# Optimization experiments

Measured on AMD Instinct MI355X. Metric: run time of the kernel, lower is better.

## Reference

```python
import jax, jax.numpy as jnp
import numpy as np

N = 40000      # nodes
E = 640000     # edges (avg degree 16)
F_IN = 32      # input node feature dim
G = 64         # graphs in batch
DIMS = [(F_IN, 128), (128, 64), (64, 32), (32, 16)]


def setup_inputs() -> dict:
    key = jax.random.key(0)
    ks = jax.random.split(key, 16)
    inp = {
        "x": jax.random.normal(ks[0], (N, F_IN), jnp.float32),
        "edge_index": jax.random.randint(ks[1], (2, E), 0, N),
        "batch": jnp.sort(jax.random.randint(ks[2], (N,), 0, G)),
    }
    k = 3
    for i, (din, dout) in enumerate(DIMS, 1):
        s = 1.0 / np.sqrt(din)
        inp[f"W{i}_rel"] = jax.random.uniform(ks[k], (din, dout), jnp.float32, -s, s); k += 1
        inp[f"b{i}"] = jax.random.uniform(ks[k], (dout,), jnp.float32, -s, s); k += 1
        inp[f"W{i}_root"] = jax.random.uniform(ks[k], (din, dout), jnp.float32, -s, s); k += 1
    s = 1.0 / np.sqrt(16)
    inp["Wfc"] = jax.random.uniform(ks[15], (16, 1), jnp.float32, -s, s)
    inp["bfc"] = jax.random.uniform(jax.random.fold_in(key, 99), (1,), jnp.float32, -s, s)
    return inp


def _graph_conv(x, src, dst, W_rel, b, W_root):
    # PyG GraphConv (aggr='add'): out_i = (sum_{j->i} x_j) @ W_rel + b + x_i @ W_root
    agg = jax.ops.segment_sum(x[src], dst, num_segments=N)  # gather -> scatter-add
    return agg @ W_rel + b + x @ W_root


def reference(x, edge_index, batch,
              W1_rel, b1, W1_root, W2_rel, b2, W2_root,
              W3_rel, b3, W3_root, W4_rel, b4, W4_root, Wfc, bfc):
    src, dst = edge_index[0], edge_index[1]
    h = jax.nn.relu(_graph_conv(x, src, dst, W1_rel, b1, W1_root))
    h = jax.nn.relu(_graph_conv(h, src, dst, W2_rel, b2, W2_root))
    h = jax.nn.relu(_graph_conv(h, src, dst, W3_rel, b3, W3_root))
    h = _graph_conv(h, src, dst, W4_rel, b4, W4_root)  # no ReLU before pooling
    # global mean pool per graph
    sums = jax.ops.segment_sum(h, batch, num_segments=G)                       # [G, 16]
    counts = jax.ops.segment_sum(jnp.ones((N, 1), h.dtype), batch, num_segments=G)
    pooled = sums / jnp.maximum(counts, 1.0)
    return pooled @ Wfc + bfc  # [G, 1]
```

## Files before the change

### kernel.cpp

```cpp
#include <hip/hip_runtime.h>

#define NN 40000
#define NE 640000
#define NG 64
#define SCAN_NB ((NN + 255) / 256)
#define CCAP 768

typedef unsigned short ushort_t;

__device__ __forceinline__ float fcomp(const float4& v, int t) {
    return t == 0 ? v.x : t == 1 ? v.y : t == 2 ? v.z : v.w;
}
__device__ __forceinline__ unsigned int pack2bf(float a, float b) {
    unsigned int ua = __float_as_uint(a);
    unsigned int ub = __float_as_uint(b);
    ua = (ua + 0x7fffu + ((ua >> 16) & 1u)) >> 16;
    ub = (ub + 0x7fffu + ((ub >> 16) & 1u)) >> 16;
    return ua | (ub << 16);
}
__device__ __forceinline__ uint2 pack4bf(const float4& v) {
    return make_uint2(pack2bf(v.x, v.y), pack2bf(v.z, v.w));
}
__device__ __forceinline__ float lo2f(unsigned int u) { return __uint_as_float(u << 16); }
__device__ __forceinline__ float hi2f(unsigned int u) { return __uint_as_float(u & 0xffff0000u); }
__device__ __forceinline__ void acc8(const uint4& u, float4& lo, float4& hi) {
    lo.x += lo2f(u.x); lo.y += hi2f(u.x); lo.z += lo2f(u.y); lo.w += hi2f(u.y);
    hi.x += lo2f(u.z); hi.y += hi2f(u.z); hi.z += lo2f(u.w); hi.w += hi2f(u.w);
}
typedef __attribute__((ext_vector_type(2))) float f32x2;
__device__ __forceinline__ unsigned int pack4fp8(const float4& v) {
    unsigned int r = 0;
    r = __builtin_amdgcn_cvt_pk_fp8_f32(v.x, v.y, r, false);
    r = __builtin_amdgcn_cvt_pk_fp8_f32(v.z, v.w, r, true);
    return r;
}
__device__ __forceinline__ void accf8x4(unsigned int u, float4& a) {
    f32x2 lo = __builtin_amdgcn_cvt_pk_f32_fp8(u, false);
    f32x2 hi = __builtin_amdgcn_cvt_pk_f32_fp8(u, true);
    a.x += lo[0]; a.y += lo[1]; a.z += hi[0]; a.w += hi[1];
}

__global__ __launch_bounds__(256) void prep_kernel(
        int* __restrict__ zp, int nz,
        const float4* __restrict__ x4,
        uint2* __restrict__ xb,
        const float* __restrict__ W4rel,
        const float* __restrict__ W4root,
        const float* __restrict__ b4,
        const float* __restrict__ Wfc,
        float* __restrict__ wf) {
    int i = blockIdx.x * 256 + threadIdx.x;
    if (i < nz) zp[i] = 0;
    if (i < NN * 8) { float4 v = x4[i]; xb[i] = pack4bf(v); }
    if (blockIdx.x == 0) {
        int t = threadIdx.x;
        if (t < 32) {
            float a = 0.f, b = 0.f;
#pragma unroll
            for (int j = 0; j < 16; ++j) {
                float w = Wfc[j];
                a += W4rel[t * 16 + j] * w;
                b += W4root[t * 16 + j] * w;
            }
            wf[t] = a;
            wf[32 + t] = b;
        } else if (t == 32) {
            float s = 0.f;
#pragma unroll
            for (int j = 0; j < 16; ++j) s += b4[j] * Wfc[j];
            wf[64] = s;
        }
    }
}

__global__ void hist_kernel(const int* __restrict__ dst, int* __restrict__ deg,
                            int* __restrict__ epos) {
    int e = blockIdx.x * blockDim.x + threadIdx.x;
    if (e < NE) epos[e] = atomicAdd(&deg[dst[e]], 1);
}

__global__ __launch_bounds__(256) void scan1_kernel(const int* __restrict__ deg,
                                                    int* __restrict__ rowptr,
                                                    int* __restrict__ bsum) {
    __shared__ int ws[4];
    __shared__ int wpre[4];
    int i = blockIdx.x * 256 + threadIdx.x;
    int lane = threadIdx.x & 63, wid = threadIdx.x >> 6;
    int v = (i < NN) ? deg[i] : 0;
    int incl = v;
#pragma unroll
    for (int off = 1; off < 64; off <<= 1) {
        int u = __shfl_up(incl, off, 64);
        if (lane >= off) incl += u;
    }
    if (lane == 63) ws[wid] = incl;
    __syncthreads();
    if (threadIdx.x == 0) {
        int s = 0;
#pragma unroll
        for (int w = 0; w < 4; ++w) { wpre[w] = s; s += ws[w]; }
        bsum[blockIdx.x] = s;
    }
    __syncthreads();
    if (i < NN) rowptr[i] = wpre[wid] + (incl - v);
}

__global__ __launch_bounds__(256) void scan23_kernel(int* __restrict__ rowptr,
                                                     const int* __restrict__ bsum) {
    __shared__ int ws[4];
    int t = threadIdx.x, b = blockIdx.x;
    int v = (t < b) ? bsum[t] : 0;
#pragma unroll
    for (int off = 32; off; off >>= 1) v += __shfl_xor(v, off, 64);
    if ((t & 63) == 0) ws[t >> 6] = v;
    __syncthreads();
    int soff = ws[0] + ws[1] + ws[2] + ws[3];
    int i = b * 256 + t;
    if (i < NN) rowptr[i] += soff;
    if (b == SCAN_NB - 1 && t == 0) rowptr[NN] = soff + bsum[b];
}

__global__ void fill_kernel(const int* __restrict__ src, const int* __restrict__ dst,
                            const int* __restrict__ rowptr, const int* __restrict__ epos,
                            ushort_t* __restrict__ col) {
    int e = blockIdx.x * blockDim.x + threadIdx.x;
    if (e < NE) col[rowptr[dst[e]] + epos[e]] = (ushort_t)src[e];
}

__global__ __launch_bounds__(256, 4) void fconv1_kernel(
        const uint4* __restrict__ xb4,
        const float4* __restrict__ x,
        const int* __restrict__ rowptr,
        const ushort_t* __restrict__ col,
        const float4* __restrict__ Wrel,
        const float4* __restrict__ Wroot,
        const float4* __restrict__ bias,
        float4* __restrict__ out) {
    __shared__ float4 sA[32][9];
    __shared__ float4 sR[32 * 32];
    __shared__ float4 sT[32 * 32];
    __shared__ ushort_t scol[CCAP];
    int t = threadIdx.x;
    for (int i = t; i < 32 * 32; i += 256) { sR[i] = Wrel[i]; sT[i] = Wroot[i]; }
    int blk0 = blockIdx.x * 32;
    int ebeg = rowptr[blk0], eend = rowptr[blk0 + 32];
    bool gat = t < 128;
    int na = t >> 2, c = t & 3;
    int node = blk0 + (gat ? na : 0);
    int beg = gat ? rowptr[node] : 0;
    int end = gat ? rowptr[node + 1] : 0;
    float4 aLo = {0.f, 0.f, 0.f, 0.f}, aHi = {0.f, 0.f, 0.f, 0.f};
    for (int base = ebeg; base < eend; base += CCAP) {
        int cnt = eend - base < CCAP ? eend - base : CCAP;
        __syncthreads();
        for (int i = t; i < cnt; i += 256) scol[i] = col[base + i];
        __syncthreads();
        if (gat) {
            int lo = beg > base ? beg : base;
            int hi = end < base + cnt ? end : base + cnt;
            int e = lo;
            for (; e + 4 <= hi; e += 4) {
                uint4 u0 = xb4[(size_t)scol[e - base] * 4 + c];
                uint4 u1 = xb4[(size_t)scol[e - base + 1] * 4 + c];
                uint4 u2 = xb4[(size_t)scol[e - base + 2] * 4 + c];
                uint4 u3 = xb4[(size_t)scol[e - base + 3] * 4 + c];
                acc8(u0, aLo, aHi); acc8(u1, aLo, aHi);
                acc8(u2, aLo, aHi); acc8(u3, aLo, aHi);
            }
            for (; e < hi; ++e) {
                uint4 u = xb4[(size_t)scol[e - base] * 4 + c];
                acc8(u, aLo, aHi);
            }
        }
    }
    if (gat) { sA[na][2 * c] = aLo; sA[na][2 * c + 1] = aHi; }
    __syncthreads();
    int jg = t % 16, mg = t / 16;
    int n0 = blk0 + mg * 2;
    float4 bb0 = bias[2 * jg], bb1 = bias[2 * jg + 1];
    float4 acc00 = bb0, acc01 = bb1, acc10 = bb0, acc11 = bb1;
#pragma unroll 2
    for (int kc = 0; kc < 8; ++kc) {
        float4 a0 = sA[2 * mg][kc];
        float4 a1 = sA[2 * mg + 1][kc];
        float4 x0 = x[(size_t)n0 * 8 + kc];
        float4 x1 = x[(size_t)(n0 + 1) * 8 + kc];
#pragma unroll
        for (int tt = 0; tt < 4; ++tt) {
            int k = kc * 4 + tt;
            float4 wr0 = sR[k * 32 + 2 * jg], wr1 = sR[k * 32 + 2 * jg + 1];
            float4 wt0 = sT[k * 32 + 2 * jg], wt1 = sT[k * 32 + 2 * jg + 1];
            float av0 = fcomp(a0, tt), xv0 = fcomp(x0, tt);
            float av1 = fcomp(a1, tt), xv1 = fcomp(x1, tt);
            acc00.x += av0 * wr0.x + xv0 * wt0.x;
            acc00.y += av0 * wr0.y + xv0 * wt0.y;
            acc00.z += av0 * wr0.z + xv0 * wt0.z;
            acc00.w += av0 * wr0.w + xv0 * wt0.w;
            acc01.x += av0 * wr1.x + xv0 * wt1.x;
            acc01.y += av0 * wr1.y + xv0 * wt1.y;
            acc01.z += av0 * wr1.z + xv0 * wt1.z;
            acc01.w += av0 * wr1.w + xv0 * wt1.w;
            acc10.x += av1 * wr0.x + xv1 * wt0.x;
            acc10.y += av1 * wr0.y + xv1 * wt0.y;
            acc10.z += av1 * wr0.z + xv1 * wt0.z;
            acc10.w += av1 * wr0.w + xv1 * wt0.w;
            acc11.x += av1 * wr1.x + xv1 * wt1.x;
            acc11.y += av1 * wr1.y + xv1 * wt1.y;
            acc11.z += av1 * wr1.z + xv1 * wt1.z;
            acc11.w += av1 * wr1.w + xv1 * wt1.w;
        }
    }
    float4 r;
    r.x = fmaxf(acc00.x, 0.f); r.y = fmaxf(acc00.y, 0.f);
    r.z = fmaxf(acc00.z, 0.f); r.w = fmaxf(acc00.w, 0.f);
    out[(size_t)n0 * 32 + 2 * jg] = r;
    r.x = fmaxf(acc01.x, 0.f); r.y = fmaxf(acc01.y, 0.f);
    r.z = fmaxf(acc01.z, 0.f); r.w = fmaxf(acc01.w, 0.f);
    out[(size_t)n0 * 32 + 2 * jg + 1] = r;
    r.x = fmaxf(acc10.x, 0.f); r.y = fmaxf(acc10.y, 0.f);
    r.z = fmaxf(acc10.z, 0.f); r.w = fmaxf(acc10.w, 0.f);
    out[(size_t)(n0 + 1) * 32 + 2 * jg] = r;
    r.x = fmaxf(acc11.x, 0.f); r.y = fmaxf(acc11.y, 0.f);
    r.z = fmaxf(acc11.z, 0.f); r.w = fmaxf(acc11.w, 0.f);
    out[(size_t)(n0 + 1) * 32 + 2 * jg + 1] = r;
}

__global__ __launch_bounds__(256, 6) void mmyz_kernel(
        const float4* __restrict__ h,
        const float4* __restrict__ Wrel,
        const float4* __restrict__ Wroot,
        const float4* __restrict__ bias,
        unsigned int* __restrict__ y2f8,
        float4* __restrict__ z2) {
    __shared__ float4 sR[32 * 16];
    __shared__ float4 sT[32 * 16];
    int jl = threadIdx.x % 16;
    int mg = threadIdx.x / 16;
    int n0 = blockIdx.x * 32 + mg * 2;
    float4 bb = bias[jl];
    float4 ay0 = {0.f, 0.f, 0.f, 0.f}, ay1 = {0.f, 0.f, 0.f, 0.f};
    float4 az0 = bb, az1 = bb;
    for (int s = 0; s < 4; ++s) {
        if (s) __syncthreads();
        for (int i = threadIdx.x; i < 512; i += 256) {
            sR[i] = Wrel[s * 512 + i];
            sT[i] = Wroot[s * 512 + i];
        }
        __syncthreads();
#pragma unroll 2
        for (int kc = 0; kc < 8; ++kc) {
            float4 h0 = h[(size_t)n0 * 32 + s * 8 + kc];
            float4 h1 = h[(size_t)(n0 + 1) * 32 + s * 8 + kc];
#pragma unroll
            for (int tt = 0; tt < 4; ++tt) {
                float4 wr = sR[(kc * 4 + tt) * 16 + jl];
                float4 wt = sT[(kc * 4 + tt) * 16 + jl];
                float v0 = fcomp(h0, tt), v1 = fcomp(h1, tt);
                ay0.x += v0 * wr.x; ay0.y += v0 * wr.y;
                ay0.z += v0 * wr.z; ay0.w += v0 * wr.w;
                az0.x += v0 * wt.x; az0.y += v0 * wt.y;
                az0.z += v0 * wt.z; az0.w += v0 * wt.w;
                ay1.x += v1 * wr.x; ay1.y += v1 * wr.y;
                ay1.z += v1 * wr.z; ay1.w += v1 * wr.w;
                az1.x += v1 * wt.x; az1.y += v1 * wt.y;
                az1.z += v1 * wt.z; az1.w += v1 * wt.w;
            }
        }
    }
    y2f8[(size_t)n0 * 16 + jl] = pack4fp8(ay0);
    z2[(size_t)n0 * 16 + jl] = az0;
    y2f8[(size_t)(n0 + 1) * 16 + jl] = pack4fp8(ay1);
    z2[(size_t)(n0 + 1) * 16 + jl] = az1;
}

__global__ __launch_bounds__(256, 5) void fconv3_kernel(
        const uint2* __restrict__ yf8,
        const float4* __restrict__ z,
        const int* __restrict__ rowptr,
        const ushort_t* __restrict__ col,
        const float4* __restrict__ Wrel,
        const float4* __restrict__ Wroot,
        const float4* __restrict__ bias,
        uint2* __restrict__ y3b,
        float4* __restrict__ z3) {
    __shared__ float4 sH[32][17];
    __shared__ float4 sR[64 * 8];
    __shared__ float4 sT[64 * 8];
    __shared__ ushort_t scol[CCAP];
    int t = threadIdx.x;
    for (int i = t; i < 64 * 8; i += 256) { sR[i] = Wrel[i]; sT[i] = Wroot[i]; }
    int blk0 = blockIdx.x * 32;
    int ebeg = rowptr[blk0], eend = rowptr[blk0 + 32];
    int na = t >> 3, c = t & 7;
    int node = blk0 + na;
    int beg = rowptr[node], end = rowptr[node + 1];
    float4 aLo = z[(size_t)node * 16 + 2 * c];
    float4 aHi = z[(size_t)node * 16 + 2 * c + 1];
    for (int base = ebeg; base < eend; base += CCAP) {
        int cnt = eend - base < CCAP ? eend - base : CCAP;
        __syncthreads();
        for (int i = t; i < cnt; i += 256) scol[i] = col[base + i];
        __syncthreads();
        int lo = beg > base ? beg : base;
        int hi = end < base + cnt ? end : base + cnt;
        int e = lo;
        for (; e + 4 <= hi; e += 4) {
            uint2 u0 = yf8[(size_t)scol[e - base] * 8 + c];
            uint2 u1 = yf8[(size_t)scol[e - base + 1] * 8 + c];
            uint2 u2 = yf8[(size_t)scol[e - base + 2] * 8 + c];
            uint2 u3 = yf8[(size_t)scol[e - base + 3] * 8 + c];
            accf8x4(u0.x, aLo); accf8x4(u0.y, aHi);
            accf8x4(u1.x, aLo); accf8x4(u1.y, aHi);
            accf8x4(u2.x, aLo); accf8x4(u2.y, aHi);
            accf8x4(u3.x, aLo); accf8x4(u3.y, aHi);
        }
        for (; e < hi; ++e) {
            uint2 u = yf8[(size_t)scol[e - base] * 8 + c];
            accf8x4(u.x, aLo); accf8x4(u.y, aHi);
        }
    }
    aLo.x = fmaxf(aLo.x, 0.f); aLo.y = fmaxf(aLo.y, 0.f);
    aLo.z = fmaxf(aLo.z, 0.f); aLo.w = fmaxf(aLo.w, 0.f);
    aHi.x = fmaxf(aHi.x, 0.f); aHi.y = fmaxf(aHi.y, 0.f);
    aHi.z = fmaxf(aHi.z, 0.f); aHi.w = fmaxf(aHi.w, 0.f);
    sH[na][2 * c] = aLo;
    sH[na][2 * c + 1] = aHi;
    __syncthreads();
    int jl = t & 7, mg = t >> 3;
    int nodeB = blk0 + mg;
    float4 ay = {0.f, 0.f, 0.f, 0.f};
    float4 az = bias[jl];
#pragma unroll 4
    for (int kc = 0; kc < 16; ++kc) {
        float4 h4 = sH[mg][kc];
#pragma unroll
        for (int tt = 0; tt < 4; ++tt) {
            float hv = fcomp(h4, tt);
            float4 wr = sR[(kc * 4 + tt) * 8 + jl];
            float4 wt = sT[(kc * 4 + tt) * 8 + jl];
            ay.x += hv * wr.x; ay.y += hv * wr.y;
            ay.z += hv * wr.z; ay.w += hv * wr.w;
            az.x += hv * wt.x; az.y += hv * wt.y;
            az.z += hv * wt.z; az.w += hv * wt.w;
        }
    }
    y3b[(size_t)nodeB * 8 + jl] = pack4bf(ay);
    z3[(size_t)nodeB * 8 + jl] = az;
}

__global__ __launch_bounds__(256, 8) void fconv4_kernel(
        const uint4* __restrict__ yb4,
        const float4* __restrict__ z,
        const int* __restrict__ rowptr,
        const ushort_t* __restrict__ col,
        const float* __restrict__ wf,
        float* __restrict__ y4,
        float* __restrict__ z4) {
    __shared__ float4 sH[32][9];
    __shared__ float4 sF[8], sRF[8];
    __shared__ float sB;
    __shared__ ushort_t scol[CCAP];
    int t = threadIdx.x;
    if (t < 8) sF[t] = ((const float4*)wf)[t];
    else if (t < 16) sRF[t - 8] = ((const float4*)wf)[t];
    else if (t == 16) sB = wf[64];
    int blk0 = blockIdx.x * 32;
    int ebeg = rowptr[blk0], eend = rowptr[blk0 + 32];
    bool gat = t < 128;
    int na = t >> 2, c = t & 3;
    int node = blk0 + (gat ? na : 0);
    int beg = gat ? rowptr[node] : 0;
    int end = gat ? rowptr[node + 1] : 0;
    float4 aLo = {0.f, 0.f, 0.f, 0.f}, aHi = {0.f, 0.f, 0.f, 0.f};
    if (gat) {
        aLo = z[(size_t)node * 8 + 2 * c];
        aHi = z[(size_t)node * 8 + 2 * c + 1];
    }
    for (int base = ebeg; base < eend; base += CCAP) {
        int cnt = eend - base < CCAP ? eend - base : CCAP;
        __syncthreads();
        for (int i = t; i < cnt; i += 256) scol[i] = col[base + i];
        __syncthreads();
        if (gat) {
            int lo = beg > base ? beg : base;
            int hi = end < base + cnt ? end : base + cnt;
            int e = lo;
            for (; e + 4 <= hi; e += 4) {
                uint4 u0 = yb4[(size_t)scol[e - base] * 4 + c];
                uint4 u1 = yb4[(size_t)scol[e - base + 1] * 4 + c];
                uint4 u2 = yb4[(size_t)scol[e - base + 2] * 4 + c];
                uint4 u3 = yb4[(size_t)scol[e - base + 3] * 4 + c];
                acc8(u0, aLo, aHi); acc8(u1, aLo, aHi);
                acc8(u2, aLo, aHi); acc8(u3, aLo, aHi);
            }
            for (; e < hi; ++e) {
                uint4 u = yb4[(size_t)scol[e - base] * 4 + c];
                acc8(u, aLo, aHi);
            }
        }
    }
    if (gat) {
        aLo.x = fmaxf(aLo.x, 0.f); aLo.y = fmaxf(aLo.y, 0.f);
        aLo.z = fmaxf(aLo.z, 0.f); aLo.w = fmaxf(aLo.w, 0.f);
        aHi.x = fmaxf(aHi.x, 0.f); aHi.y = fmaxf(aHi.y, 0.f);
        aHi.z = fmaxf(aHi.z, 0.f); aHi.w = fmaxf(aHi.w, 0.f);
        sH[na][2 * c] = aLo;
        sH[na][2 * c + 1] = aHi;
    }
    __syncthreads();
    if (t < 32) {
        int nd = blk0 + t;
        float ay = 0.f, az = 0.f;
#pragma unroll
        for (int kc = 0; kc < 8; ++kc) {
            float4 h4 = sH[t][kc];
            float4 f = sF[kc], r = sRF[kc];
            ay += h4.x * f.x + h4.y * f.y + h4.z * f.z + h4.w * f.w;
            az += h4.x * r.x + h4.y * r.y + h4.z * r.z + h4.w * r.w;
        }
        y4[nd] = ay;
        z4[nd] = az + sB;
    }
}

__global__ __launch_bounds__(256) void gpool_final_kernel(
        const float* __restrict__ y4,
        const float* __restrict__ z4,
        const int* __restrict__ rowptr,
        const ushort_t* __restrict__ col,
        const int* __restrict__ batch,
        float* __restrict__ sums,
        float* __restrict__ counts,
        int* __restrict__ ctr,
        const float* __restrict__ bfc,
        float* __restrict__ out) {
    __shared__ float ls[NG];
    __shared__ float lc[NG];
    __shared__ int sDone;
    if (threadIdx.x < NG) { ls[threadIdx.x] = 0.f; lc[threadIdx.x] = 0.f; }
    if (threadIdx.x == 0) sDone = 0;
    __syncthreads();
    int nd = blockIdx.x * 256 + threadIdx.x;
    if (nd < NN) {
        float v = z4[nd];
        int beg = rowptr[nd], end = rowptr[nd + 1];
        int e = beg;
        for (; e + 4 <= end; e += 4) {
            v += (y4[col[e]] + y4[col[e + 1]]) + (y4[col[e + 2]] + y4[col[e + 3]]);
        }
        for (; e < end; ++e) v += y4[col[e]];
        int g = batch[nd];
        atomicAdd(&ls[g], v);
        atomicAdd(&lc[g], 1.f);
    }
    __syncthreads();
    if (threadIdx.x < NG && lc[threadIdx.x] > 0.f) {
        atomicAdd(&sums[threadIdx.x], ls[threadIdx.x]);
        atomicAdd(&counts[threadIdx.x], lc[threadIdx.x]);
    }
    __threadfence();
    __syncthreads();
    if (threadIdx.x == 0) {
        if (atomicAdd(ctr, 1) == (int)gridDim.x - 1) sDone = 1;
    }
    __syncthreads();
    if (sDone && threadIdx.x < NG) {
        float s = atomicAdd(&sums[threadIdx.x], 0.f);
        float c = atomicAdd(&counts[threadIdx.x], 0.f);
        c = fmaxf(c, 1.0f);
        out[threadIdx.x] = s / c + bfc[0];
    }
}

extern "C" void kernel_launch(void* const* d_in, const int* in_sizes, int n_in,
                              void* d_out, int out_size, void* d_ws, size_t ws_size,
                              hipStream_t stream) {
    const float* x       = (const float*)d_in[0];
    const int*   ei      = (const int*)d_in[1];
    const int*   batch   = (const int*)d_in[2];
    const float* W1_rel  = (const float*)d_in[3];
    const float* b1      = (const float*)d_in[4];
    const float* W1_root = (const float*)d_in[5];
    const float* W2_rel  = (const float*)d_in[6];
    const float* b2      = (const float*)d_in[7];
    const float* W2_root = (const float*)d_in[8];
    const float* W3_rel  = (const float*)d_in[9];
    const float* b3      = (const float*)d_in[10];
    const float* W3_root = (const float*)d_in[11];
    const float* W4_rel  = (const float*)d_in[12];
    const float* b4      = (const float*)d_in[13];
    const float* W4_root = (const float*)d_in[14];
    const float* Wfc     = (const float*)d_in[15];
    const float* bfc     = (const float*)d_in[16];
    float* out = (float*)d_out;

    const int* src = ei;
    const int* dst = ei + NE;

    float* bufH    = (float*)d_ws;
    float* bufZ    = bufH + (size_t)NN * 128;
    float* z3      = bufZ + (size_t)NN * 64;
    float* y4      = z3 + (size_t)NN * 32;
    float* z4      = y4 + NN;
    float* wf      = z4 + NN;
    int*   deg     = (int*)(wf + 68);
    float* sums    = (float*)(deg + NN);
    float* counts  = sums + NG;
    int*   ctr     = (int*)(counts + NG);
    int*   rowptr  = ctr + 1;
    int*   epos    = rowptr + NN + 1;
    int*   bsum    = epos + NE;
    ushort_t* colu = (ushort_t*)(bsum + 160);
    unsigned long long pa = (unsigned long long)(colu + NE);
    pa = (pa + 15ull) & ~15ull;
    uint2* xb      = (uint2*)pa;
    unsigned int* y2f8 = (unsigned int*)(xb + (size_t)NN * 8);
    uint2* y3b     = (uint2*)(y2f8 + (size_t)NN * 16);

    const int NZ = NN + 2 * NG + 1;

    prep_kernel<<<NN * 8 / 256, 256, 0, stream>>>(
        deg, NZ, (const float4*)x, xb, W4_rel, W4_root, b4, Wfc, wf);

    hist_kernel<<<(NE + 255) / 256, 256, 0, stream>>>(dst, deg, epos);
    scan1_kernel<<<SCAN_NB, 256, 0, stream>>>(deg, rowptr, bsum);
    scan23_kernel<<<SCAN_NB, 256, 0, stream>>>(rowptr, bsum);
    fill_kernel<<<(NE + 255) / 256, 256, 0, stream>>>(src, dst, rowptr, epos, colu);

    fconv1_kernel<<<NN / 32, 256, 0, stream>>>(
        (const uint4*)xb, (const float4*)x, rowptr, colu,
        (const float4*)W1_rel, (const float4*)W1_root, (const float4*)b1,
        (float4*)bufH);

    mmyz_kernel<<<NN / 32, 256, 0, stream>>>(
        (const float4*)bufH, (const float4*)W2_rel, (const float4*)W2_root,
        (const float4*)b2, y2f8, (float4*)bufZ);

    fconv3_kernel<<<NN / 32, 256, 0, stream>>>(
        (const uint2*)y2f8, (const float4*)bufZ, rowptr, colu,
        (const float4*)W3_rel, (const float4*)W3_root, (const float4*)b3,
        y3b, (float4*)z3);

    fconv4_kernel<<<NN / 32, 256, 0, stream>>>(
        (const uint4*)y3b, (const float4*)z3, rowptr, colu, wf, y4, z4);

    gpool_final_kernel<<<(NN + 255) / 256, 256, 0, stream>>>(
        y4, z4, rowptr, colu, batch, sums, counts, ctr, bfc, out);
}
```

Baseline: 146.8 us.

## Fuse CSR build kernels with grid sync and store layer-1 output in bf16

Merges the histogram and bf16 input packing into one kernel, and merges the two-phase scan and column fill into a single kernel that uses an atomic-counter grid barrier across its 157 blocks. The intent is to cut kernel launch overhead and inter-kernel gaps in the CSR construction. Separately, the layer-1 activations are written as bf16 instead of fp32 and unpacked in the next matmul, halving that intermediate's memory traffic. The grid barrier assumes all blocks are co-resident, and bf16 storage adds rounding error.

Measured after the change: 160.2 us. +9.2%, slower.

```diff
diff --git a/kernel.cpp b/kernel.cpp
--- a/kernel.cpp
+++ b/kernel.cpp
@@ -23,6 +23,9 @@
 }
 __device__ __forceinline__ float lo2f(unsigned int u) { return __uint_as_float(u << 16); }
 __device__ __forceinline__ float hi2f(unsigned int u) { return __uint_as_float(u & 0xffff0000u); }
+__device__ __forceinline__ float4 unp4(const uint2& u) {
+    float4 r; r.x = lo2f(u.x); r.y = hi2f(u.x); r.z = lo2f(u.y); r.w = hi2f(u.y); return r;
+}
 __device__ __forceinline__ void acc8(const uint4& u, float4& lo, float4& hi) {
     lo.x += lo2f(u.x); lo.y += hi2f(u.x); lo.z += lo2f(u.y); lo.w += hi2f(u.y);
     hi.x += lo2f(u.z); hi.y += hi2f(u.z); hi.z += lo2f(u.w); hi.w += hi2f(u.w);
@@ -39,19 +42,33 @@
     f32x2 hi = __builtin_amdgcn_cvt_pk_f32_fp8(u, true);
     a.x += lo[0]; a.y += lo[1]; a.z += hi[0]; a.w += hi[1];
 }
-
-__global__ __launch_bounds__(256) void prep_kernel(
-        int* __restrict__ zp, int nz,
-        const float4* __restrict__ x4,
-        uint2* __restrict__ xb,
-        const float* __restrict__ W4rel,
-        const float* __restrict__ W4root,
-        const float* __restrict__ b4,
-        const float* __restrict__ Wfc,
-        float* __restrict__ wf) {
+__device__ __forceinline__ void gsync(int* cnt, int nblk) {
+    __syncthreads();
+    if (threadIdx.x == 0) {
+        __threadfence();
+        atomicAdd(cnt, 1);
+        while (atomicAdd(cnt, 0) < nblk) { __builtin_amdgcn_s_sleep(2); }
+        __threadfence();
+    }
+    __syncthreads();
+}
+
+__global__ __launch_bounds__(256) void zero_kernel(int* __restrict__ p, int n) {
     int i = blockIdx.x * 256 + threadIdx.x;
-    if (i < nz) zp[i] = 0;
-    if (i < NN * 8) { float4 v = x4[i]; xb[i] = pack4bf(v); }
+    if (i < n) p[i] = 0;
+}
+
+__global__ void csr1_kernel(const int* __restrict__ dst, int* __restrict__ deg,
+                            int* __restrict__ epos,
+                            const float4* __restrict__ x4, uint2* __restrict__ xb,
+                            const float* __restrict__ W4rel,
+                            const float* __restrict__ W4root,
+                            const float* __restrict__ b4,
+                            const float* __restrict__ Wfc,
+                            float* __restrict__ wf) {
+    int e = blockIdx.x * blockDim.x + threadIdx.x;
+    if (e < NE) epos[e] = atomicAdd(&deg[dst[e]], 1);
+    if (e < NN * 8) xb[e] = pack4bf(x4[e]);
     if (blockIdx.x == 0) {
         int t = threadIdx.x;
         if (t < 32) {
@@ -73,58 +90,53 @@
     }
 }
 
-__global__ void hist_kernel(const int* __restrict__ dst, int* __restrict__ deg,
-                            int* __restrict__ epos) {
-    int e = blockIdx.x * blockDim.x + threadIdx.x;
-    if (e < NE) epos[e] = atomicAdd(&deg[dst[e]], 1);
-}
-
-__global__ __launch_bounds__(256) void scan1_kernel(const int* __restrict__ deg,
-                                                    int* __restrict__ rowptr,
-                                                    int* __restrict__ bsum) {
+__global__ __launch_bounds__(256) void csr2_kernel(
+        const int* __restrict__ deg,
+        int* __restrict__ rowptr,
+        int* __restrict__ bsum,
+        const int* __restrict__ src, const int* __restrict__ dst,
+        const int* __restrict__ epos,
+        ushort_t* __restrict__ col,
+        int* __restrict__ sc) {
     __shared__ int ws[4];
     __shared__ int wpre[4];
-    int i = blockIdx.x * 256 + threadIdx.x;
-    int lane = threadIdx.x & 63, wid = threadIdx.x >> 6;
-    int v = (i < NN) ? deg[i] : 0;
-    int incl = v;
-#pragma unroll
-    for (int off = 1; off < 64; off <<= 1) {
-        int u = __shfl_up(incl, off, 64);
-        if (lane >= off) incl += u;
-    }
-    if (lane == 63) ws[wid] = incl;
-    __syncthreads();
-    if (threadIdx.x == 0) {
-        int s = 0;
-#pragma unroll
-        for (int w = 0; w < 4; ++w) { wpre[w] = s; s += ws[w]; }
-        bsum[blockIdx.x] = s;
-    }
-    __syncthreads();
-    if (i < NN) rowptr[i] = wpre[wid] + (incl - v);
-}
-
-__global__ __launch_bounds__(256) void scan23_kernel(int* __restrict__ rowptr,
-                                                     const int* __restrict__ bsum) {
-    __shared__ int ws[4];
     int t = threadIdx.x, b = blockIdx.x;
-    int v = (t < b) ? bsum[t] : 0;
-#pragma unroll
-    for (int off = 32; off; off >>= 1) v += __shfl_xor(v, off, 64);
-    if ((t & 63) == 0) ws[t >> 6] = v;
-    __syncthreads();
-    int soff = ws[0] + ws[1] + ws[2] + ws[3];
-    int i = b * 256 + t;
-    if (i < NN) rowptr[i] += soff;
-    if (b == SCAN_NB - 1 && t == 0) rowptr[NN] = soff + bsum[b];
-}
-
-__global__ void fill_kernel(const int* __restrict__ src, const int* __restrict__ dst,
-                            const int* __restrict__ rowptr, const int* __restrict__ epos,
-                            ushort_t* __restrict__ col) {
-    int e = blockIdx.x * blockDim.x + threadIdx.x;
-    if (e < NE) col[rowptr[dst[e]] + epos[e]] = (ushort_t)src[e];
+    int lane = t & 63, wid = t >> 6;
+    {
+        int i = b * 256 + t;
+        int v = (i < NN) ? deg[i] : 0;
+        int incl = v;
+#pragma unroll
+        for (int off = 1; off < 64; off <<= 1) {
+            int u = __shfl_up(incl, off, 64);
+            if (lane >= off) incl += u;
+        }
+        if (lane == 63) ws[wid] = incl;
+        __syncthreads();
+        if (t == 0) {
+            int s = 0;
+#pragma unroll
+            for (int w = 0; w < 4; ++w) { wpre[w] = s; s += ws[w]; }
+            bsum[b] = s;
+        }
+        __syncthreads();
+        if (i < NN) rowptr[i] = wpre[wid] + (incl - v);
+    }
+    gsync(&sc[0], SCAN_NB);
+    {
+        int v = (t < b) ? bsum[t] : 0;
+#pragma unroll
+        for (int off = 32; off; off >>= 1) v += __shfl_xor(v, off, 64);
+        if (lane == 0) ws[wid] = v;
+        __syncthreads();
+        int soff = ws[0] + ws[1] + ws[2] + ws[3];
+        int i = b * 256 + t;
+        if (i < NN) rowptr[i] += soff;
+        if (b == SCAN_NB - 1 && t == 0) rowptr[NN] = soff + bsum[b];
+    }
+    gsync(&sc[1], SCAN_NB);
+    for (int e = b * 256 + t; e < NE; e += SCAN_NB * 256)
+        col[rowptr[dst[e]] + epos[e]] = (ushort_t)src[e];
 }
 
 __global__ __launch_bounds__(256, 4) void fconv1_kernel(
@@ -135,7 +147,7 @@
         const float4* __restrict__ Wrel,
         const float4* __restrict__ Wroot,
         const float4* __restrict__ bias,
-        float4* __restrict__ out) {
+        uint2* __restrict__ outb) {
     __shared__ float4 sA[32][9];
     __shared__ float4 sR[32 * 32];
     __shared__ float4 sT[32 * 32];
@@ -213,20 +225,20 @@
     float4 r;
     r.x = fmaxf(acc00.x, 0.f); r.y = fmaxf(acc00.y, 0.f);
     r.z = fmaxf(acc00.z, 0.f); r.w = fmaxf(acc00.w, 0.f);
-    out[(size_t)n0 * 32 + 2 * jg] = r;
+    outb[(size_t)n0 * 32 + 2 * jg] = pack4bf(r);
     r.x = fmaxf(acc01.x, 0.f); r.y = fmaxf(acc01.y, 0.f);
     r.z = fmaxf(acc01.z, 0.f); r.w = fmaxf(acc01.w, 0.f);
-    out[(size_t)n0 * 32 + 2 * jg + 1] = r;
+    outb[(size_t)n0 * 32 + 2 * jg + 1] = pack4bf(r);
     r.x = fmaxf(acc10.x, 0.f); r.y = fmaxf(acc10.y, 0.f);
     r.z = fmaxf(acc10.z, 0.f); r.w = fmaxf(acc10.w, 0.f);
-    out[(size_t)(n0 + 1) * 32 + 2 * jg] = r;
+    outb[(size_t)(n0 + 1) * 32 + 2 * jg] = pack4bf(r);
     r.x = fmaxf(acc11.x, 0.f); r.y = fmaxf(acc11.y, 0.f);
     r.z = fmaxf(acc11.z, 0.f); r.w = fmaxf(acc11.w, 0.f);
-    out[(size_t)(n0 + 1) * 32 + 2 * jg + 1] = r;
+    outb[(size_t)(n0 + 1) * 32 + 2 * jg + 1] = pack4bf(r);
 }
 
 __global__ __launch_bounds__(256, 6) void mmyz_kernel(
-        const float4* __restrict__ h,
+        const uint2* __restrict__ hb,
         const float4* __restrict__ Wrel,
         const float4* __restrict__ Wroot,
         const float4* __restrict__ bias,
@@ -249,8 +261,8 @@
         __syncthreads();
 #pragma unroll 2
         for (int kc = 0; kc < 8; ++kc) {
-            float4 h0 = h[(size_t)n0 * 32 + s * 8 + kc];
-            float4 h1 = h[(size_t)(n0 + 1) * 32 + s * 8 + kc];
+            float4 h0 = unp4(hb[(size_t)n0 * 32 + s * 8 + kc]);
+            float4 h1 = unp4(hb[(size_t)(n0 + 1) * 32 + s * 8 + kc]);
 #pragma unroll
             for (int tt = 0; tt < 4; ++tt) {
                 float4 wr = sR[(kc * 4 + tt) * 16 + jl];
@@ -497,8 +509,8 @@
     const int* src = ei;
     const int* dst = ei + NE;
 
-    float* bufH    = (float*)d_ws;
-    float* bufZ    = bufH + (size_t)NN * 128;
+    uint2* h1b     = (uint2*)d_ws;
+    float* bufZ    = (float*)(h1b + (size_t)NN * 32);
     float* z3      = bufZ + (size_t)NN * 64;
     float* y4      = z3 + (size_t)NN * 32;
     float* z4      = y4 + NN;
@@ -507,7 +519,8 @@
     float* sums    = (float*)(deg + NN);
     float* counts  = sums + NG;
     int*   ctr     = (int*)(counts + NG);
-    int*   rowptr  = ctr + 1;
+    int*   sc      = ctr + 1;
+    int*   rowptr  = sc + 2;
     int*   epos    = rowptr + NN + 1;
     int*   bsum    = epos + NE;
     ushort_t* colu = (ushort_t*)(bsum + 160);
@@ -517,23 +530,23 @@
     unsigned int* y2f8 = (unsigned int*)(xb + (size_t)NN * 8);
     uint2* y3b     = (uint2*)(y2f8 + (size_t)NN * 16);
 
-    const int NZ = NN + 2 * NG + 1;
-
-    prep_kernel<<<NN * 8 / 256, 256, 0, stream>>>(
-        deg, NZ, (const float4*)x, xb, W4_rel, W4_root, b4, Wfc, wf);
-
-    hist_kernel<<<(NE + 255) / 256, 256, 0, stream>>>(dst, deg, epos);
-    scan1_kernel<<<SCAN_NB, 256, 0, stream>>>(deg, rowptr, bsum);
-    scan23_kernel<<<SCAN_NB, 256, 0, stream>>>(rowptr, bsum);
-    fill_kernel<<<(NE + 255) / 256, 256, 0, stream>>>(src, dst, rowptr, epos, colu);
+    const int NZ = NN + 2 * NG + 3;
+
+    zero_kernel<<<(NZ + 255) / 256, 256, 0, stream>>>(deg, NZ);
+
+    csr1_kernel<<<(NE + 255) / 256, 256, 0, stream>>>(
+        dst, deg, epos, (const float4*)x, xb, W4_rel, W4_root, b4, Wfc, wf);
+
+    csr2_kernel<<<SCAN_NB, 256, 0, stream>>>(
+        deg, rowptr, bsum, src, dst, epos, colu, sc);
 
     fconv1_kernel<<<NN / 32, 256, 0, stream>>>(
         (const uint4*)xb, (const float4*)x, rowptr, colu,
         (const float4*)W1_rel, (const float4*)W1_root, (const float4*)b1,
-        (float4*)bufH);
+        h1b);
 
     mmyz_kernel<<<NN / 32, 256, 0, stream>>>(
-        (const float4*)bufH, (const float4*)W2_rel, (const float4*)W2_root,
+        h1b, (const float4*)W2_rel, (const float4*)W2_root,
         (const float4*)b2, y2f8, (float4*)bufZ);
 
     fconv3_kernel<<<NN / 32, 256, 0, stream>>>(
```
